# Optimization experiments

Measured on AMD Instinct MI355X. Metric: run time of the kernel, lower is better.

Reference implementation:

```python
import jax, jax.numpy as jnp
import numpy as np
import math

N_NODES = 50000
N_EDGES = 1600000
DIM = 64
HEADS = 8
EDGE_DIM = 32


def setup_inputs() -> dict:
    key = jax.random.key(0)
    ks = jax.random.split(key, 12)
    s = 1.0 / math.sqrt(DIM)
    se = 1.0 / math.sqrt(EDGE_DIM)
    return {
        'x': jax.random.normal(ks[0], (N_NODES, DIM), jnp.float32),
        'edge_index': jax.random.randint(ks[1], (2, N_EDGES), 0, N_NODES),
        'edge_attr': jax.random.normal(ks[2], (N_EDGES, EDGE_DIM), jnp.float32),
        'WQ': jax.random.normal(ks[3], (DIM, DIM), jnp.float32) * s,
        'bQ': jnp.zeros((DIM,), jnp.float32),
        'WK': jax.random.normal(ks[4], (DIM, DIM), jnp.float32) * s,
        'bK': jnp.zeros((DIM,), jnp.float32),
        'WV': jax.random.normal(ks[5], (DIM, DIM), jnp.float32) * s,
        'bV': jnp.zeros((DIM,), jnp.float32),
        'WO': jax.random.normal(ks[6], (DIM, DIM), jnp.float32) * s,
        'bO': jnp.zeros((DIM,), jnp.float32),
        'We1': jax.random.normal(ks[7], (EDGE_DIM, EDGE_DIM), jnp.float32) * se,
        'be1': jnp.zeros((EDGE_DIM,), jnp.float32),
        'We2': jax.random.normal(ks[8], (EDGE_DIM, HEADS), jnp.float32) * se,
        'be2': jnp.zeros((HEADS,), jnp.float32),
    }


def graph_softmax(src, index, num_segments):
    # src: [E, H], index: [E] -> per-destination-node stable softmax
    smax = jax.ops.segment_max(src, index, num_segments=num_segments)  # [N, H]
    smax = jnp.where(jnp.isfinite(smax), smax, 0.0)  # nodes with no edges
    e = jnp.exp(src - smax[index])
    ssum = jax.ops.segment_sum(e, index, num_segments=num_segments) + 1e-12
    return e / ssum[index]


def reference(x, edge_index, edge_attr, WQ, bQ, WK, bK, WV, bV, WO, bO, We1, be1, We2, be2):
    num_nodes = x.shape[0]
    d_k = DIM // HEADS
    i, j = edge_index[0], edge_index[1]
    # per-node projections [N, H, d_k], then gather per-edge
    Q = (x @ WQ + bQ).reshape(num_nodes, HEADS, d_k)
    K = (x @ WK + bK).reshape(num_nodes, HEADS, d_k)
    V = (x @ WV + bV).reshape(num_nodes, HEADS, d_k)
    query = Q[j]  # [E, H, d_k]
    key = K[i]
    value = V[i]
    # edge bias MLP: [edge_dim -> edge_dim -> num_heads] with SiLU between
    h = jax.nn.silu(edge_attr @ We1 + be1)
    bias = h @ We2 + be2  # [E, H]
    scores = jnp.sum(query * key, axis=-1) / math.sqrt(d_k) + bias  # [E, H]
    alpha = graph_softmax(scores, j, num_nodes)  # [E, H]
    weighted = (alpha[..., None] * value).reshape(-1, DIM)  # [E, dim]
    attn_out = jax.ops.segment_sum(weighted, j, num_segments=num_nodes)  # [N, dim]
    return attn_out @ WO + bO
```

## Files before the change

### kernel.cpp

```cpp
#include <hip/hip_runtime.h>
#include <math.h>

#define N_NODES 50000
#define N_EDGES 1600000
#define DIM 64
#define HEADS 8
#define EDGE_DIM 32

#define NB 256
#define NPB 196
#define ACAP 8192
#define PART_T 256
#define EPT 8
#define PART_E (PART_T * EPT)

#define QKV_BLKS 12500

typedef __fp16 h2 __attribute__((ext_vector_type(2)));

__device__ __forceinline__ unsigned int f2bf(float f) {
    union { float f; unsigned int u; } c; c.f = f;
    unsigned int u = c.u;
    return (u + 0x7FFFu + ((u >> 16) & 1u)) >> 16;
}
__device__ __forceinline__ float bf_lo(unsigned int u) { return __uint_as_float(u << 16); }
__device__ __forceinline__ float bf_hi(unsigned int u) { return __uint_as_float(u & 0xFFFF0000u); }
__device__ __forceinline__ unsigned int h2u(h2 v) { union { h2 h; unsigned int u; } c; c.h = v; return c.u; }
__device__ __forceinline__ h2 u2h(unsigned int x) { union { h2 h; unsigned int u; } c; c.u = x; return c.h; }

__global__ __launch_bounds__(1024) void pack_weights(
    const float* __restrict__ We1, const float* __restrict__ We2,
    h2* __restrict__ w1p, h2* __restrict__ w2p, int* __restrict__ gcur)
{
    const int t = threadIdx.x;
    if (t < 512) {
        const int c = t >> 4, kk = t & 15;
        w1p[t] = __builtin_amdgcn_cvt_pkrtz(We1[(2 * kk) * EDGE_DIM + c],
                                            We1[(2 * kk + 1) * EDGE_DIM + c]);
    } else if (t < 512 + 128) {
        const int u = t - 512;
        const int h = u >> 4, cc = u & 15;
        w2p[u] = __builtin_amdgcn_cvt_pkrtz(We2[(2 * cc) * HEADS + h],
                                            We2[(2 * cc + 1) * HEADS + h]);
    } else if (t >= 768 && t < 768 + NB) {
        gcur[t - 768] = 0;
    }
}

__global__ __launch_bounds__(256) void mlp_only(
    const float* __restrict__ edge_attr,
    const h2* __restrict__ w1p, const float* __restrict__ be1,
    const h2* __restrict__ w2p, const float* __restrict__ be2,
    uint4* __restrict__ bias_by_e)
{
    const int e = blockIdx.x * 256 + threadIdx.x;
    if (e >= N_EDGES) return;
    float a[EDGE_DIM];
    const float4* ar = (const float4*)(edge_attr + (size_t)e * EDGE_DIM);
    #pragma unroll
    for (int q = 0; q < EDGE_DIM / 4; ++q) {
        float4 v = ar[q];
        a[q * 4 + 0] = v.x; a[q * 4 + 1] = v.y;
        a[q * 4 + 2] = v.z; a[q * 4 + 3] = v.w;
    }
    h2 a2[EDGE_DIM / 2];
    #pragma unroll
    for (int kk = 0; kk < EDGE_DIM / 2; ++kk)
        a2[kk] = __builtin_amdgcn_cvt_pkrtz(a[2 * kk], a[2 * kk + 1]);
    float sil[EDGE_DIM];
    #pragma unroll 8
    for (int c = 0; c < EDGE_DIM; ++c) {
        float s = be1[c];
        #pragma unroll
        for (int kk = 0; kk < EDGE_DIM / 2; ++kk)
            s = __builtin_amdgcn_fdot2(a2[kk], w1p[c * 16 + kk], s, false);
        sil[c] = __fdividef(s, 1.0f + __expf(-s));
    }
    h2 s2[EDGE_DIM / 2];
    #pragma unroll
    for (int cc = 0; cc < EDGE_DIM / 2; ++cc)
        s2[cc] = __builtin_amdgcn_cvt_pkrtz(sil[2 * cc], sil[2 * cc + 1]);
    float b0f = be2[0], b1f = be2[1], b2f = be2[2], b3f = be2[3];
    float b4f = be2[4], b5f = be2[5], b6f = be2[6], b7f = be2[7];
    #pragma unroll
    for (int cc = 0; cc < EDGE_DIM / 2; ++cc) {
        b0f = __builtin_amdgcn_fdot2(s2[cc], w2p[0 * 16 + cc], b0f, false);
        b1f = __builtin_amdgcn_fdot2(s2[cc], w2p[1 * 16 + cc], b1f, false);
        b2f = __builtin_amdgcn_fdot2(s2[cc], w2p[2 * 16 + cc], b2f, false);
        b3f = __builtin_amdgcn_fdot2(s2[cc], w2p[3 * 16 + cc], b3f, false);
        b4f = __builtin_amdgcn_fdot2(s2[cc], w2p[4 * 16 + cc], b4f, false);
        b5f = __builtin_amdgcn_fdot2(s2[cc], w2p[5 * 16 + cc], b5f, false);
        b6f = __builtin_amdgcn_fdot2(s2[cc], w2p[6 * 16 + cc], b6f, false);
        b7f = __builtin_amdgcn_fdot2(s2[cc], w2p[7 * 16 + cc], b7f, false);
    }
    uint4 br;
    br.x = f2bf(b0f) | (f2bf(b1f) << 16);
    br.y = f2bf(b2f) | (f2bf(b3f) << 16);
    br.z = f2bf(b4f) | (f2bf(b5f) << 16);
    br.w = f2bf(b6f) | (f2bf(b7f) << 16);
    bias_by_e[e] = br;
}

__global__ __launch_bounds__(256) void partition_only(
    const int* __restrict__ ei, int* __restrict__ gcur, uint2* __restrict__ A_rec)
{
    __shared__ int cnt[NB];
    __shared__ int base[NB];
    __shared__ int lbase[NB];
    __shared__ int total_s;
    __shared__ uint2 srec[PART_E];
    __shared__ unsigned char sbkt[PART_E];
    const int tid = threadIdx.x;
    cnt[tid] = 0;
    __syncthreads();
    const int e0 = blockIdx.x * PART_E;
    #pragma unroll
    for (int k = 0; k < EPT; ++k) {
        const int e = e0 + k * PART_T + tid;
        if (e < N_EDGES) atomicAdd(&cnt[ei[N_EDGES + e] / NPB], 1);
    }
    __syncthreads();
    lbase[tid] = cnt[tid];
    __syncthreads();
    for (int o = 1; o < NB; o <<= 1) {
        int t = (tid >= o) ? lbase[tid - o] : 0;
        __syncthreads();
        lbase[tid] += t;
        __syncthreads();
    }
    {
        const int inc = lbase[tid];
        const int c = cnt[tid];
        base[tid] = (c > 0) ? atomicAdd(&gcur[tid], c) : 0;
        lbase[tid] = inc - c;
        if (tid == NB - 1) total_s = inc;
        cnt[tid] = 0;
    }
    __syncthreads();
    #pragma unroll
    for (int k = 0; k < EPT; ++k) {
        const int e = e0 + k * PART_T + tid;
        if (e < N_EDGES) {
            const int i = ei[e];
            const int j = ei[N_EDGES + e];
            const int b = j / NPB;
            const int jl = j - b * NPB;
            const int s = lbase[b] + atomicAdd(&cnt[b], 1);
            srec[s] = make_uint2((unsigned)e, ((unsigned)jl << 24) | (unsigned)i);
            sbkt[s] = (unsigned char)b;
        }
    }
    __syncthreads();
    const int total = total_s;
    for (int s = tid; s < total; s += PART_T) {
        const int b = sbkt[s];
        const int gp = base[b] + (s - lbase[b]);
        if (gp < ACAP) A_rec[(size_t)b * ACAP + gp] = srec[s];
    }
}

__global__ __launch_bounds__(256) void perm_qkv(
    const int* __restrict__ gcur, const uint2* __restrict__ A_rec,
    int* __restrict__ offs, uint2* __restrict__ es_sorted,
    const float* __restrict__ x,
    const float* __restrict__ WQ, const float* __restrict__ bQ,
    const float* __restrict__ WK, const float* __restrict__ bK,
    const float* __restrict__ WV, const float* __restrict__ bV,
    unsigned int* __restrict__ Q2, unsigned int* __restrict__ KV2)
{
    __shared__ __align__(16) char smem[3 * DIM * DIM * sizeof(float)];
    const int tid = threadIdx.x;
    if (blockIdx.x < NB) {
        int* sc   = (int*)smem;
        int* ldeg = sc + NB;
        int* loff = ldeg + NPB;
        int* gb   = loff + NPB + 1;
        const int b = blockIdx.x;
        sc[tid] = min(gcur[tid], ACAP);
        __syncthreads();
        for (int o = 1; o < NB; o <<= 1) {
            int t = (tid >= o) ? sc[tid - o] : 0;
            __syncthreads();
            sc[tid] += t;
            __syncthreads();
        }
        if (tid == 0) gb[0] = (b == 0) ? 0 : sc[b - 1];
        if (tid < NPB) ldeg[tid] = 0;
        __syncthreads();
        const int gbase = gb[0];
        const int nb = min(gcur[b], ACAP);
        for (int r = tid; r < nb; r += 256)
            atomicAdd(&ldeg[A_rec[(size_t)b * ACAP + r].y >> 24], 1);
        __syncthreads();
        sc[tid] = (tid < NPB) ? ldeg[tid] : 0;
        __syncthreads();
        for (int o = 1; o < 256; o <<= 1) {
            int t = (tid >= o) ? sc[tid - o] : 0;
            __syncthreads();
            sc[tid] += t;
            __syncthreads();
        }
        if (tid == 0) loff[0] = 0;
        if (tid < NPB) { loff[tid + 1] = sc[tid]; ldeg[tid] = 0; }
        __syncthreads();
        const int jbase = b * NPB;
        if (tid < NPB && jbase + tid < N_NODES) offs[jbase + tid] = gbase + loff[tid];
        if (b == NB - 1 && tid == 0) offs[N_NODES] = gbase + nb;
        for (int r = tid; r < nb; r += 256) {
            const uint2 rec = A_rec[(size_t)b * ACAP + r];
            const int jl = (int)(rec.y >> 24);
            const int slot = loff[jl] + atomicAdd(&ldeg[jl], 1);
            es_sorted[(size_t)gbase + slot] = make_uint2(rec.x, rec.y & 0xFFFFFFu);
        }
    } else {
        float* sWQ = (float*)smem;
        float* sWK = sWQ + DIM * DIM;
        float* sWV = sWK + DIM * DIM;
        for (int t = tid; t < DIM * DIM; t += 256) {
            sWQ[t] = WQ[t]; sWK[t] = WK[t]; sWV[t] = WV[t];
        }
        __syncthreads();
        const int lane = tid & 63;
        const int wave = tid >> 6;
        const int n = (blockIdx.x - NB) * 4 + wave;
        if (n >= N_NODES) return;
        float xl = x[(size_t)n * DIM + lane];
        float aq = bQ[lane], ak = bK[lane], av = bV[lane];
        #pragma unroll
        for (int k = 0; k < DIM; ++k) {
            float xv = __shfl(xl, k, 64);
            aq += xv * sWQ[k * DIM + lane];
            ak += xv * sWK[k * DIM + lane];
            av += xv * sWV[k * DIM + lane];
        }
        const int s = lane & 31;
        const float aq_e = __shfl(aq, 2 * s, 64);
        const float aq_o = __shfl(aq, 2 * s + 1, 64);
        const float ak_e = __shfl(ak, 2 * s, 64);
        const float ak_o = __shfl(ak, 2 * s + 1, 64);
        const float av_e = __shfl(av, 2 * s, 64);
        const float av_o = __shfl(av, 2 * s + 1, 64);
        if (lane < 32) {
            Q2[(size_t)n * 32 + s]  = h2u(__builtin_amdgcn_cvt_pkrtz(aq_e, aq_o));
            KV2[(size_t)n * 64 + s] = h2u(__builtin_amdgcn_cvt_pkrtz(ak_e, ak_o));
        } else {
            KV2[(size_t)n * 64 + 32 + s] = f2bf(av_e) | (f2bf(av_o) << 16);
        }
    }
}

__global__ __launch_bounds__(256) void node_attn_out(
    const int* __restrict__ off,
    const uint2* __restrict__ es_sorted,
    const unsigned short* __restrict__ bias_u16,
    const unsigned int* __restrict__ Q2, const unsigned int* __restrict__ KV2,
    const float* __restrict__ WO, const float* __restrict__ bO,
    float* __restrict__ out)
{
    __shared__ float sWO[DIM * DIM];
    for (int t = threadIdx.x; t < DIM * DIM; t += 256) sWO[t] = WO[t];
    __syncthreads();
    const int lane = threadIdx.x & 63;
    const int wave = threadIdx.x >> 6;
    const int j = blockIdx.x * 4 + wave;
    if (j >= N_NODES) return;
    const int beg = off[j], end = off[j + 1];
    const int s = lane & 31;
    const int half = lane >> 5;
    const int h = s >> 2;
    const float inv_sqrt_dk = 0.35355339059327373f;
    const h2 q2 = u2h(Q2[(size_t)j * 32 + s]);
    float num2x = 0.0f, num2y = 0.0f;
    float den = 1e-12f;
    int t = beg;
    for (; t + 7 < end; t += 8) {
        uint2 r[4];
        unsigned int k2v[4], v2v[4];
        float bb[4], d[4];
        #pragma unroll
        for (int q = 0; q < 4; ++q) r[q] = es_sorted[t + 2 * q + half];
        #pragma unroll
        for (int q = 0; q < 4; ++q) k2v[q] = KV2[(size_t)r[q].y * 64 + s];
        #pragma unroll
        for (int q = 0; q < 4; ++q) v2v[q] = KV2[(size_t)r[q].y * 64 + 32 + s];
        #pragma unroll
        for (int q = 0; q < 4; ++q)
            bb[q] = bf_lo((unsigned int)bias_u16[(size_t)r[q].x * HEADS + h]);
        #pragma unroll
        for (int q = 0; q < 4; ++q)
            d[q] = __builtin_amdgcn_fdot2(q2, u2h(k2v[q]), 0.0f, false);
        #pragma unroll
        for (int q = 0; q < 4; ++q) d[q] += __shfl_xor(d[q], 1, 64);
        #pragma unroll
        for (int q = 0; q < 4; ++q) d[q] += __shfl_xor(d[q], 2, 64);
        #pragma unroll
        for (int q = 0; q < 4; ++q) {
            const float ev = __expf(d[q] * inv_sqrt_dk + bb[q]);
            num2x += ev * bf_lo(v2v[q]);
            num2y += ev * bf_hi(v2v[q]);
            den += ev;
        }
    }
    for (; t + 1 < end; t += 2) {
        const uint2 r0 = es_sorted[t + half];
        const unsigned int k2v = KV2[(size_t)r0.y * 64 + s];
        const unsigned int v2v = KV2[(size_t)r0.y * 64 + 32 + s];
        const float bb = bf_lo((unsigned int)bias_u16[(size_t)r0.x * HEADS + h]);
        float d = __builtin_amdgcn_fdot2(q2, u2h(k2v), 0.0f, false);
        d += __shfl_xor(d, 1, 64);
        d += __shfl_xor(d, 2, 64);
        const float ev = __expf(d * inv_sqrt_dk + bb);
        num2x += ev * bf_lo(v2v);
        num2y += ev * bf_hi(v2v);
        den += ev;
    }
    if (t < end) {
        const uint2 r0 = es_sorted[t];
        const unsigned int k2v = KV2[(size_t)r0.y * 64 + s];
        const unsigned int v2v = KV2[(size_t)r0.y * 64 + 32 + s];
        const float bb = bf_lo((unsigned int)bias_u16[(size_t)r0.x * HEADS + h]);
        float d = __builtin_amdgcn_fdot2(q2, u2h(k2v), 0.0f, false);
        d += __shfl_xor(d, 1, 64);
        d += __shfl_xor(d, 2, 64);
        float ev = __expf(d * inv_sqrt_dk + bb);
        if (half != 0) ev = 0.0f;
        num2x += ev * bf_lo(v2v);
        num2y += ev * bf_hi(v2v);
        den += ev;
    }
    num2x += __shfl_xor(num2x, 32, 64);
    num2y += __shfl_xor(num2y, 32, 64);
    den   += __shfl_xor(den, 32, 64);
    const float av2x = num2x / den;
    const float av2y = num2y / den;
    float acc = bO[lane];
    #pragma unroll
    for (int sp = 0; sp < 32; ++sp) {
        acc += __shfl(av2x, sp, 64) * sWO[(2 * sp) * DIM + lane];
        acc += __shfl(av2y, sp, 64) * sWO[(2 * sp + 1) * DIM + lane];
    }
    out[(size_t)j * DIM + lane] = acc;
}

extern "C" void kernel_launch(void* const* d_in, const int* in_sizes, int n_in,
                              void* d_out, int out_size, void* d_ws, size_t ws_size,
                              hipStream_t stream) {
    const float* x    = (const float*)d_in[0];
    const int*   ei   = (const int*)d_in[1];
    const float* ea   = (const float*)d_in[2];
    const float* WQ   = (const float*)d_in[3];
    const float* bQ   = (const float*)d_in[4];
    const float* WK   = (const float*)d_in[5];
    const float* bK   = (const float*)d_in[6];
    const float* WV   = (const float*)d_in[7];
    const float* bV   = (const float*)d_in[8];
    const float* WO   = (const float*)d_in[9];
    const float* bO   = (const float*)d_in[10];
    const float* We1  = (const float*)d_in[11];
    const float* be1  = (const float*)d_in[12];
    const float* We2  = (const float*)d_in[13];
    const float* be2  = (const float*)d_in[14];
    float* out = (float*)d_out;

    char* ws = (char*)d_ws;
    size_t off_b = 0;
    auto alloc = [&](size_t bytes) {
        void* p = ws + off_b;
        off_b += (bytes + 255) & ~(size_t)255;
        return p;
    };
    unsigned int* Q2        = (unsigned int*)alloc((size_t)N_NODES * 32 * sizeof(unsigned int));
    unsigned int* KV2       = (unsigned int*)alloc((size_t)N_NODES * 64 * sizeof(unsigned int));
    uint2*        A_rec     = (uint2*)alloc((size_t)NB * ACAP * sizeof(uint2));
    uint4*        bias_by_e = (uint4*)alloc((size_t)N_EDGES * sizeof(uint4));
    uint2*        es_sorted = (uint2*)alloc((size_t)N_EDGES * sizeof(uint2));
    int*          offs      = (int*)alloc((size_t)(N_NODES + 1) * sizeof(int));
    int*          gcur      = (int*)alloc((size_t)NB * sizeof(int));
    h2*           w1p       = (h2*)alloc(512 * sizeof(h2));
    h2*           w2p       = (h2*)alloc(128 * sizeof(h2));

    pack_weights<<<1, 1024, 0, stream>>>(We1, We2, w1p, w2p, gcur);
    partition_only<<<(N_EDGES + PART_E - 1) / PART_E, PART_T, 0, stream>>>(ei, gcur, A_rec);
    mlp_only<<<(N_EDGES + 255) / 256, 256, 0, stream>>>(ea, w1p, be1, w2p, be2, bias_by_e);
    perm_qkv<<<NB + QKV_BLKS, 256, 0, stream>>>(gcur, A_rec, offs, es_sorted,
                                                x, WQ, bQ, WK, bK, WV, bV, Q2, KV2);
    node_attn_out<<<(N_NODES + 3) / 4, 256, 0, stream>>>(offs, es_sorted,
                                                         (const unsigned short*)bias_by_e,
                                                         Q2, KV2, WO, bO, out);
}
```

Baseline: 291.6 us.

## Permute edge bias into destination-sorted order and use wave-shuffle scans

Measured after the change: 303.4 us. 1.04x slower.

```diff
diff --git a/kernel.cpp b/kernel.cpp
--- a/kernel.cpp
+++ b/kernel.cpp
@@ -107,10 +107,13 @@
     __shared__ int cnt[NB];
     __shared__ int base[NB];
     __shared__ int lbase[NB];
+    __shared__ int wsum[4];
     __shared__ int total_s;
     __shared__ uint2 srec[PART_E];
     __shared__ unsigned char sbkt[PART_E];
     const int tid = threadIdx.x;
+    const int lane = tid & 63;
+    const int w = tid >> 6;
     cnt[tid] = 0;
     __syncthreads();
     const int e0 = blockIdx.x * PART_E;
@@ -120,20 +123,23 @@
         if (e < N_EDGES) atomicAdd(&cnt[ei[N_EDGES + e] / NPB], 1);
     }
     __syncthreads();
-    lbase[tid] = cnt[tid];
-    __syncthreads();
-    for (int o = 1; o < NB; o <<= 1) {
-        int t = (tid >= o) ? lbase[tid - o] : 0;
-        __syncthreads();
-        lbase[tid] += t;
-        __syncthreads();
-    }
+    int v = cnt[tid];
+    #pragma unroll
+    for (int o = 1; o < 64; o <<= 1) {
+        int t = __shfl_up(v, o, 64);
+        if (lane >= o) v += t;
+    }
+    if (lane == 63) wsum[w] = v;
+    __syncthreads();
+    int add = 0;
+    #pragma unroll
+    for (int ww = 0; ww < 3; ++ww) if (ww < w) add += wsum[ww];
+    v += add;
     {
-        const int inc = lbase[tid];
         const int c = cnt[tid];
         base[tid] = (c > 0) ? atomicAdd(&gcur[tid], c) : 0;
-        lbase[tid] = inc - c;
-        if (tid == NB - 1) total_s = inc;
+        lbase[tid] = v - c;
+        if (tid == NB - 1) total_s = v;
         cnt[tid] = 0;
     }
     __syncthreads();
@@ -161,7 +167,9 @@
 
 __global__ __launch_bounds__(256) void perm_qkv(
     const int* __restrict__ gcur, const uint2* __restrict__ A_rec,
-    int* __restrict__ offs, uint2* __restrict__ es_sorted,
+    const uint4* __restrict__ bias_by_e,
+    int* __restrict__ offs, int* __restrict__ src_sorted,
+    uint4* __restrict__ bias_sorted,
     const float* __restrict__ x,
     const float* __restrict__ WQ, const float* __restrict__ bQ,
     const float* __restrict__ WK, const float* __restrict__ bK,
@@ -170,21 +178,21 @@
 {
     __shared__ __align__(16) char smem[3 * DIM * DIM * sizeof(float)];
     const int tid = threadIdx.x;
+    const int lane = tid & 63;
+    const int w = tid >> 6;
     if (blockIdx.x < NB) {
-        int* sc   = (int*)smem;
-        int* ldeg = sc + NB;
+        int* ldeg = (int*)smem;
         int* loff = ldeg + NPB;
-        int* gb   = loff + NPB + 1;
+        int* wsum = loff + NPB + 1;
+        int* gb   = wsum + 4;
         const int b = blockIdx.x;
-        sc[tid] = min(gcur[tid], ACAP);
-        __syncthreads();
-        for (int o = 1; o < NB; o <<= 1) {
-            int t = (tid >= o) ? sc[tid - o] : 0;
-            __syncthreads();
-            sc[tid] += t;
-            __syncthreads();
-        }
-        if (tid == 0) gb[0] = (b == 0) ? 0 : sc[b - 1];
+        if (w == 0) {
+            int ssum = 0;
+            for (int t = lane; t < b; t += 64) ssum += min(gcur[t], ACAP);
+            #pragma unroll
+            for (int o = 1; o < 64; o <<= 1) ssum += __shfl_xor(ssum, o, 64);
+            if (lane == 0) gb[0] = ssum;
+        }
         if (tid < NPB) ldeg[tid] = 0;
         __syncthreads();
         const int gbase = gb[0];
@@ -192,16 +200,20 @@
         for (int r = tid; r < nb; r += 256)
             atomicAdd(&ldeg[A_rec[(size_t)b * ACAP + r].y >> 24], 1);
         __syncthreads();
-        sc[tid] = (tid < NPB) ? ldeg[tid] : 0;
+        int v = (tid < NPB) ? ldeg[tid] : 0;
+        #pragma unroll
+        for (int o = 1; o < 64; o <<= 1) {
+            int t = __shfl_up(v, o, 64);
+            if (lane >= o) v += t;
+        }
+        if (lane == 63) wsum[w] = v;
         __syncthreads();
-        for (int o = 1; o < 256; o <<= 1) {
-            int t = (tid >= o) ? sc[tid - o] : 0;
-            __syncthreads();
-            sc[tid] += t;
-            __syncthreads();
-        }
+        int add = 0;
+        #pragma unroll
+        for (int ww = 0; ww < 3; ++ww) if (ww < w) add += wsum[ww];
+        v += add;
         if (tid == 0) loff[0] = 0;
-        if (tid < NPB) { loff[tid + 1] = sc[tid]; ldeg[tid] = 0; }
+        if (tid < NPB) { loff[tid + 1] = v; ldeg[tid] = 0; }
         __syncthreads();
         const int jbase = b * NPB;
         if (tid < NPB && jbase + tid < N_NODES) offs[jbase + tid] = gbase + loff[tid];
@@ -210,7 +222,9 @@
             const uint2 rec = A_rec[(size_t)b * ACAP + r];
             const int jl = (int)(rec.y >> 24);
             const int slot = loff[jl] + atomicAdd(&ldeg[jl], 1);
-            es_sorted[(size_t)gbase + slot] = make_uint2(rec.x, rec.y & 0xFFFFFFu);
+            const int gp = gbase + slot;
+            src_sorted[gp] = (int)(rec.y & 0xFFFFFFu);
+            bias_sorted[gp] = bias_by_e[rec.x];
         }
     } else {
         float* sWQ = (float*)smem;
@@ -220,9 +234,7 @@
             sWQ[t] = WQ[t]; sWK[t] = WK[t]; sWV[t] = WV[t];
         }
         __syncthreads();
-        const int lane = tid & 63;
-        const int wave = tid >> 6;
-        const int n = (blockIdx.x - NB) * 4 + wave;
+        const int n = (blockIdx.x - NB) * 4 + w;
         if (n >= N_NODES) return;
         float xl = x[(size_t)n * DIM + lane];
         float aq = bQ[lane], ak = bK[lane], av = bV[lane];
@@ -251,7 +263,7 @@
 
 __global__ __launch_bounds__(256) void node_attn_out(
     const int* __restrict__ off,
-    const uint2* __restrict__ es_sorted,
+    const int* __restrict__ src_sorted,
     const unsigned short* __restrict__ bias_u16,
     const unsigned int* __restrict__ Q2, const unsigned int* __restrict__ KV2,
     const float* __restrict__ WO, const float* __restrict__ bO,
@@ -274,18 +286,18 @@
     float den = 1e-12f;
     int t = beg;
     for (; t + 7 < end; t += 8) {
-        uint2 r[4];
+        int iv[4];
         unsigned int k2v[4], v2v[4];
         float bb[4], d[4];
         #pragma unroll
-        for (int q = 0; q < 4; ++q) r[q] = es_sorted[t + 2 * q + half];
-        #pragma unroll
-        for (int q = 0; q < 4; ++q) k2v[q] = KV2[(size_t)r[q].y * 64 + s];
-        #pragma unroll
-        for (int q = 0; q < 4; ++q) v2v[q] = KV2[(size_t)r[q].y * 64 + 32 + s];
+        for (int q = 0; q < 4; ++q) iv[q] = src_sorted[t + 2 * q + half];
+        #pragma unroll
+        for (int q = 0; q < 4; ++q) k2v[q] = KV2[(size_t)iv[q] * 64 + s];
+        #pragma unroll
+        for (int q = 0; q < 4; ++q) v2v[q] = KV2[(size_t)iv[q] * 64 + 32 + s];
         #pragma unroll
         for (int q = 0; q < 4; ++q)
-            bb[q] = bf_lo((unsigned int)bias_u16[(size_t)r[q].x * HEADS + h]);
+            bb[q] = bf_lo((unsigned int)bias_u16[(size_t)(t + 2 * q + half) * HEADS + h]);
         #pragma unroll
         for (int q = 0; q < 4; ++q)
             d[q] = __builtin_amdgcn_fdot2(q2, u2h(k2v[q]), 0.0f, false);
@@ -302,10 +314,10 @@
         }
     }
     for (; t + 1 < end; t += 2) {
-        const uint2 r0 = es_sorted[t + half];
-        const unsigned int k2v = KV2[(size_t)r0.y * 64 + s];
-        const unsigned int v2v = KV2[(size_t)r0.y * 64 + 32 + s];
-        const float bb = bf_lo((unsigned int)bias_u16[(size_t)r0.x * HEADS + h]);
+        const int iv = src_sorted[t + half];
+        const unsigned int k2v = KV2[(size_t)iv * 64 + s];
+        const unsigned int v2v = KV2[(size_t)iv * 64 + 32 + s];
+        const float bb = bf_lo((unsigned int)bias_u16[(size_t)(t + half) * HEADS + h]);
         float d = __builtin_amdgcn_fdot2(q2, u2h(k2v), 0.0f, false);
         d += __shfl_xor(d, 1, 64);
         d += __shfl_xor(d, 2, 64);
@@ -315,10 +327,10 @@
         den += ev;
     }
     if (t < end) {
-        const uint2 r0 = es_sorted[t];
-        const unsigned int k2v = KV2[(size_t)r0.y * 64 + s];
-        const unsigned int v2v = KV2[(size_t)r0.y * 64 + 32 + s];
-        const float bb = bf_lo((unsigned int)bias_u16[(size_t)r0.x * HEADS + h]);
+        const int iv = src_sorted[t];
+        const unsigned int k2v = KV2[(size_t)iv * 64 + s];
+        const unsigned int v2v = KV2[(size_t)iv * 64 + 32 + s];
+        const float bb = bf_lo((unsigned int)bias_u16[(size_t)t * HEADS + h]);
         float d = __builtin_amdgcn_fdot2(q2, u2h(k2v), 0.0f, false);
         d += __shfl_xor(d, 1, 64);
         d += __shfl_xor(d, 2, 64);
@@ -369,22 +381,24 @@
         off_b += (bytes + 255) & ~(size_t)255;
         return p;
     };
-    unsigned int* Q2        = (unsigned int*)alloc((size_t)N_NODES * 32 * sizeof(unsigned int));
-    unsigned int* KV2       = (unsigned int*)alloc((size_t)N_NODES * 64 * sizeof(unsigned int));
-    uint2*        A_rec     = (uint2*)alloc((size_t)NB * ACAP * sizeof(uint2));
-    uint4*        bias_by_e = (uint4*)alloc((size_t)N_EDGES * sizeof(uint4));
-    uint2*        es_sorted = (uint2*)alloc((size_t)N_EDGES * sizeof(uint2));
-    int*          offs      = (int*)alloc((size_t)(N_NODES + 1) * sizeof(int));
-    int*          gcur      = (int*)alloc((size_t)NB * sizeof(int));
-    h2*           w1p       = (h2*)alloc(512 * sizeof(h2));
-    h2*           w2p       = (h2*)alloc(128 * sizeof(h2));
+    unsigned int* Q2          = (unsigned int*)alloc((size_t)N_NODES * 32 * sizeof(unsigned int));
+    unsigned int* KV2         = (unsigned int*)alloc((size_t)N_NODES * 64 * sizeof(unsigned int));
+    uint2*        A_rec       = (uint2*)alloc((size_t)NB * ACAP * sizeof(uint2));
+    uint4*        bias_by_e   = (uint4*)alloc((size_t)N_EDGES * sizeof(uint4));
+    uint4*        bias_sorted = (uint4*)alloc((size_t)N_EDGES * sizeof(uint4));
+    int*          src_sorted  = (int*)alloc((size_t)N_EDGES * sizeof(int));
+    int*          offs        = (int*)alloc((size_t)(N_NODES + 1) * sizeof(int));
+    int*          gcur        = (int*)alloc((size_t)NB * sizeof(int));
+    h2*           w1p         = (h2*)alloc(512 * sizeof(h2));
+    h2*           w2p         = (h2*)alloc(128 * sizeof(h2));
 
     pack_weights<<<1, 1024, 0, stream>>>(We1, We2, w1p, w2p, gcur);
     partition_only<<<(N_EDGES + PART_E - 1) / PART_E, PART_T, 0, stream>>>(ei, gcur, A_rec);
     mlp_only<<<(N_EDGES + 255) / 256, 256, 0, stream>>>(ea, w1p, be1, w2p, be2, bias_by_e);
-    perm_qkv<<<NB + QKV_BLKS, 256, 0, stream>>>(gcur, A_rec, offs, es_sorted,
+    perm_qkv<<<NB + QKV_BLKS, 256, 0, stream>>>(gcur, A_rec, bias_by_e,
+                                                offs, src_sorted, bias_sorted,
                                                 x, WQ, bQ, WK, bK, WV, bV, Q2, KV2);
-    node_attn_out<<<(N_NODES + 3) / 4, 256, 0, stream>>>(offs, es_sorted,
-                                                         (const unsigned short*)bias_by_e,
+    node_attn_out<<<(N_NODES + 3) / 4, 256, 0, stream>>>(offs, src_sorted,
+                                                         (const unsigned short*)bias_sorted,
                                                          Q2, KV2, WO, bO, out);
 }
```
